# Kernel tuning notes

Measured on AMD Instinct MI355X. Metric: run time of the kernel, lower is better.

Reference implementation:

```python
import jax, jax.numpy as jnp
import numpy as np

B, N, HID, H = 2, 2048, 2048, 16
DH = HID // H  # 128


def _rope_tables(n, d, base=10000.0):
    inv_freq = 1.0 / (base ** (np.arange(0, d, 2, dtype=np.float32) / d))
    t = np.arange(n, dtype=np.float32)
    freqs = np.outer(t, inv_freq)                 # [N, d/2]
    emb = np.concatenate([freqs, freqs], axis=-1)  # [N, d]
    return jnp.asarray(np.cos(emb)), jnp.asarray(np.sin(emb))


def setup_inputs() -> dict:
    key = jax.random.key(0)
    k1, k2, k3 = jax.random.split(key, 3)
    std = 1.0 / HID ** 0.5
    cos, sin = _rope_tables(N, DH)
    return {
        "hidden_states": jax.random.normal(k1, (B, N, HID), dtype=jnp.float32),
        "cos": cos,
        "sin": sin,
        "w_qkv": (jax.random.truncated_normal(k2, -2.0, 2.0, (3 * HID, HID), jnp.float32) * std),
        "w_o": (jax.random.truncated_normal(k3, -2.0, 2.0, (HID, HID), jnp.float32) * std),
    }


def _rotate_half(x):
    d = x.shape[-1] // 2
    return jnp.concatenate([-x[..., d:], x[..., :d]], axis=-1)


def reference(hidden_states, cos, sin, w_qkv, w_o):
    b, n, _ = hidden_states.shape
    qkv = (hidden_states @ w_qkv.T).reshape(b, n, 3, H, DH)
    q, k, v = qkv[:, :, 0], qkv[:, :, 1], qkv[:, :, 2]  # [B,N,H,DH]
    c = cos[:, None, :]  # [N,1,DH] broadcasts over heads
    s = sin[:, None, :]
    q = q * c + _rotate_half(q) * s
    k = k * c + _rotate_half(k) * s
    scale = 1.0 / jnp.sqrt(jnp.asarray(DH, q.dtype))
    scores = jnp.einsum("bqhd,bkhd->bhqk", q, k) * scale
    attn = jax.nn.softmax(scores, axis=-1)
    out = jnp.einsum("bhqk,bkhd->bqhd", attn, v).reshape(b, n, HID)
    return out @ w_o.T
```

## Files before the change

### kernel.cpp

```cpp
#include <hip/hip_runtime.h>
#include <math.h>

#define NB 2
#define NN 2048
#define HIDDEN 2048
#define NHEAD 16
#define DHEAD 128

typedef __attribute__((ext_vector_type(8))) short bf16x8;
typedef __attribute__((ext_vector_type(4))) float floatx4;

static __device__ __forceinline__ short f2bf(float f) {
    union { float f; unsigned u; } v; v.f = f;
    unsigned r = v.u + 0x7fffu + ((v.u >> 16) & 1u);
    return (short)(r >> 16);
}
static __device__ __forceinline__ void gload_lds16(const short* g, short* l) {
    __builtin_amdgcn_global_load_lds(
        (const __attribute__((address_space(1))) void*)g,
        (__attribute__((address_space(3))) void*)l, 16, 0, 0);
}

__global__ __launch_bounds__(256) void cast_bf16_3(
    const float* __restrict__ a, const float* __restrict__ b, const float* __restrict__ c,
    short* __restrict__ oa, short* __restrict__ ob, short* __restrict__ oc,
    int n4a, int n4b, int n4c)
{
    int i = blockIdx.x * 256 + threadIdx.x;
    const float* s; short* d; int j;
    if (i < n4a) { s = a; d = oa; j = i; }
    else if (i < n4a + n4b) { s = b; d = ob; j = i - n4a; }
    else if (i < n4a + n4b + n4c) { s = c; d = oc; j = i - n4a - n4b; }
    else return;
    float4 v = ((const float4*)s)[j];
    short4 o;
    o.x = f2bf(v.x); o.y = f2bf(v.y); o.z = f2bf(v.z); o.w = f2bf(v.w);
    ((short4*)d)[j] = o;
}

__global__ __launch_bounds__(512, 2) void gemm_qkv_256x128(
    const short* __restrict__ A, const short* __restrict__ Bw,
    const float* __restrict__ cosT, const float* __restrict__ sinT,
    short* __restrict__ Qp, short* __restrict__ Kp, short* __restrict__ Vtp)
{
    __shared__ __align__(16) short AB[49152];

    const int tid = threadIdx.x;
    const int w = tid >> 6;
    const int l = tid & 63;
    const int quad = l >> 4;
    const int l15 = l & 15;
    const int bn = blockIdx.x * 128;
    const int bm = blockIdx.y * 256;
    const int K = HIDDEN;

    const short* src[6];
    int ldst[6];
#pragma unroll
    for (int ld = 0; ld < 2; ++ld) {
        int chunk = ld * 512 + tid;
        int row = chunk >> 3;
        int j = (chunk & 7) ^ (row & 7);
        int coff = j * 8;
        src[ld]     = A + (size_t)(bm + row) * K + coff;
        src[2 + ld] = A + (size_t)(bm + 128 + row) * K + coff;
        ldst[ld]     = chunk * 16;
        ldst[2 + ld] = 16384 + chunk * 16;
    }
    {
        int row = tid >> 3;
        int j = (tid & 7) ^ (row & 7);
        int coff = j * 8;
        src[4] = Bw + (size_t)(bn + row) * K + coff;
        src[5] = Bw + (size_t)(bn + 64 + row) * K + coff;
        ldst[4] = 32768 + tid * 16;
        ldst[5] = 32768 + 8192 + tid * 16;
    }

    const int xj = l15 & 7;
    const int jq0 = ((0 * 4 + quad) ^ xj) * 16;
    const int jq1 = ((1 * 4 + quad) ^ xj) * 16;
    const int arow = (w * 32 + l15) * 128;
    const int brow = 32768 + l15 * 128;

    floatx4 acc[2][8];
#pragma unroll
    for (int i = 0; i < 2; ++i)
#pragma unroll
        for (int j = 0; j < 8; ++j) acc[i][j] = (floatx4){0.f, 0.f, 0.f, 0.f};

#pragma unroll
    for (int i = 0; i < 6; ++i)
        gload_lds16(src[i], (short*)((char*)AB + ldst[i]));

#define STAGE(i) gload_lds16(src[i] + kpf, (short*)((char*)AB + ldst[i] + so))
#define MFMA(d, x, y) d = __builtin_amdgcn_mfma_f32_16x16x32_bf16(x, y, d, 0, 0, 0)

    const int NT = K / 64;
#pragma unroll 1
    for (int t = 0; t < NT; ++t) {
        const int co = (t & 1) * 49152;
        const int so = co ^ 49152;
        int kpf = (t + 1) * 64;
        if (kpf == K) kpf = 0;

        bf16x8 a[2][2], b[4][2];

        asm volatile("s_waitcnt vmcnt(1)" ::: "memory");
        __builtin_amdgcn_s_barrier();
#pragma unroll
        for (int m = 0; m < 2; ++m) {
            a[m][0] = *(const bf16x8*)((const char*)AB + co + arow + m * 2048 + jq0);
            a[m][1] = *(const bf16x8*)((const char*)AB + co + arow + m * 2048 + jq1);
        }
#pragma unroll
        for (int n = 0; n < 4; ++n) {
            b[n][0] = *(const bf16x8*)((const char*)AB + co + brow + n * 2048 + jq0);
            b[n][1] = *(const bf16x8*)((const char*)AB + co + brow + n * 2048 + jq1);
        }
        STAGE(0); STAGE(1); STAGE(2); STAGE(3); STAGE(4);
        __builtin_amdgcn_s_setprio(1);
#pragma unroll
        for (int m = 0; m < 2; ++m)
#pragma unroll
            for (int n = 0; n < 4; ++n) {
                MFMA(acc[m][n], a[m][0], b[n][0]);
                MFMA(acc[m][n], a[m][1], b[n][1]);
            }
        __builtin_amdgcn_s_setprio(0);

        asm volatile("s_waitcnt vmcnt(5)" ::: "memory");
        __builtin_amdgcn_s_barrier();
#pragma unroll
        for (int n = 0; n < 4; ++n) {
            b[n][0] = *(const bf16x8*)((const char*)AB + co + brow + (4 + n) * 2048 + jq0);
            b[n][1] = *(const bf16x8*)((const char*)AB + co + brow + (4 + n) * 2048 + jq1);
        }
        STAGE(5);
        __builtin_amdgcn_s_setprio(1);
#pragma unroll
        for (int m = 0; m < 2; ++m)
#pragma unroll
            for (int n = 0; n < 4; ++n) {
                MFMA(acc[m][4 + n], a[m][0], b[n][0]);
                MFMA(acc[m][4 + n], a[m][1], b[n][1]);
            }
        __builtin_amdgcn_s_setprio(0);
    }
#undef STAGE
#undef MFMA

    asm volatile("s_waitcnt vmcnt(0)" ::: "memory");

    const int which = bn >> 11;
    const int head = (bn >> 7) & (NHEAD - 1);
    const float qsc = (which == 0) ? 0.12751791525f : 1.0f;

#pragma unroll
    for (int m = 0; m < 2; ++m) {
#pragma unroll
        for (int reg = 0; reg < 4; ++reg) {
            int gm = bm + w * 32 + m * 16 + quad * 4 + reg;
            int b2 = gm >> 11, nseq = gm & (NN - 1);
            int bh = b2 * NHEAD + head;
            if (which == 2) {
#pragma unroll
                for (int n = 0; n < 8; ++n) {
                    int d = n * 16 + l15;
                    Vtp[((size_t)bh * DHEAD + d) * NN + nseq] = f2bf(acc[m][n][reg]);
                }
            } else {
                short* dst = (which == 0 ? Qp : Kp) + ((size_t)bh * NN + nseq) * DHEAD;
#pragma unroll
                for (int p = 0; p < 4; ++p) {
                    int d0 = p * 16 + l15;
                    float c = cosT[(size_t)nseq * DHEAD + d0];
                    float s = sinT[(size_t)nseq * DHEAD + d0];
                    float e0 = acc[m][p][reg];
                    float e1 = acc[m][p + 4][reg];
                    dst[d0]      = f2bf((e0 * c - e1 * s) * qsc);
                    dst[d0 + 64] = f2bf((e1 * c + e0 * s) * qsc);
                }
            }
        }
    }
}

template <int MODE>
__global__ __launch_bounds__(256) void gemm_bf16_nt(
    const short* __restrict__ A, const short* __restrict__ Bw,
    const float* __restrict__ cosT, const float* __restrict__ sinT,
    short* __restrict__ Qp, short* __restrict__ Kp, short* __restrict__ Vtp,
    float* __restrict__ Cp, int M, int N, int K)
{
    __shared__ __align__(16) short AB[1280 * 8];

    const int tid = threadIdx.x;
    const int w = tid >> 6;
    const int l = tid & 63;
    const int quad = l >> 4;
    const int l15 = l & 15;
    const int bm = blockIdx.y * 128;
    const int bn = blockIdx.x * 128;

    const int wm = (w & 1) * 64;
    const int wn2 = w >> 1;

    const short* gptr[5];
    short* lptr[5];
#pragma unroll
    for (int r5 = 0; r5 < 5; ++r5) {
        int s = r5 * 256 + tid;
        int m = (s < 640) ? s : s - 640;
        int row = m / 5;
        int ch = m - row * 5;
        if (ch == 4) ch = 0;
        gptr[r5] = ((s < 640) ? (A + (size_t)(bm + row) * K)
                              : (Bw + (size_t)(bn + row) * K)) + ch * 8;
        lptr[r5] = &AB[s * 8];
    }

    floatx4 acc[4][4];
#pragma unroll
    for (int i = 0; i < 4; ++i)
#pragma unroll
        for (int j = 0; j < 4; ++j) acc[i][j] = (floatx4){0.f, 0.f, 0.f, 0.f};

    for (int k0 = 0; k0 < K; k0 += 32) {
        __syncthreads();
#pragma unroll
        for (int r5 = 0; r5 < 5; ++r5)
            gload_lds16(gptr[r5] + k0, lptr[r5]);
        __syncthreads();

        bf16x8 af[4], bf[4];
#pragma unroll
        for (int i = 0; i < 4; ++i)
            af[i] = *(const bf16x8*)&AB[((wm + i * 16 + l15) * 5 + quad) * 8];
#pragma unroll
        for (int j = 0; j < 4; ++j) {
            int col = wn2 * 32 + (j & 1) * 16 + ((j >> 1) << 6);
            bf[j] = *(const bf16x8*)&AB[(640 + (col + l15) * 5 + quad) * 8];
        }
#pragma unroll
        for (int i = 0; i < 4; ++i)
#pragma unroll
            for (int j = 0; j < 4; ++j)
                acc[i][j] = __builtin_amdgcn_mfma_f32_16x16x32_bf16(af[i], bf[j], acc[i][j], 0, 0, 0);
    }

    if (MODE == 1) {
#pragma unroll
        for (int i = 0; i < 4; ++i) {
#pragma unroll
            for (int reg = 0; reg < 4; ++reg) {
                int row = bm + wm + i * 16 + quad * 4 + reg;
                float* crow = Cp + (size_t)row * N + bn;
#pragma unroll
                for (int j = 0; j < 4; ++j)
                    crow[wn2 * 32 + (j & 1) * 16 + ((j >> 1) << 6) + l15] = acc[i][j][reg];
            }
        }
    } else {
        const int which = bn >> 11;
        const int head = (bn >> 7) & (NHEAD - 1);
        const float qsc = (which == 0) ? 0.12751791525f : 1.0f;
#pragma unroll
        for (int i = 0; i < 4; ++i) {
#pragma unroll
            for (int reg = 0; reg < 4; ++reg) {
                int m = bm + wm + i * 16 + quad * 4 + reg;
                int b = m >> 11, n = m & (NN - 1);
                int bh = b * NHEAD + head;
                if (which == 2) {
#pragma unroll
                    for (int j = 0; j < 4; ++j) {
                        int d = wn2 * 32 + (j & 1) * 16 + ((j >> 1) << 6) + l15;
                        Vtp[((size_t)bh * DHEAD + d) * NN + n] = f2bf(acc[i][j][reg]);
                    }
                } else {
                    short* dst = (which == 0 ? Qp : Kp) + ((size_t)bh * NN + n) * DHEAD;
#pragma unroll
                    for (int j = 0; j < 2; ++j) {
                        int d0 = wn2 * 32 + j * 16 + l15;
                        float c = cosT[(size_t)n * DHEAD + d0];
                        float s = sinT[(size_t)n * DHEAD + d0];
                        float e0 = acc[i][j][reg], e1 = acc[i][j + 2][reg];
                        dst[d0]      = f2bf((e0 * c - e1 * s) * qsc);
                        dst[d0 + 64] = f2bf((e1 * c + e0 * s) * qsc);
                    }
                }
            }
        }
    }
}

__global__ __launch_bounds__(256, 2) void attn_mfma(
    const short* __restrict__ Qb, const short* __restrict__ Kb,
    const short* __restrict__ Vt, short* __restrict__ AOb)
{
    __shared__ __align__(16) short Ks[64 * 128];
    __shared__ __align__(16) short Vs[128 * 64];
    __shared__ __align__(16) short Ps[4][32][72];

    const int tid = threadIdx.x;
    const int w = tid >> 6;
    const int l = tid & 63;
    const int quad = l >> 4;
    const int l15 = l & 15;
    const int bh = blockIdx.y;
    const int qt = blockIdx.x * 128;

    const short* Qg = Qb + (size_t)bh * NN * DHEAD;
    const short* Kg = Kb + (size_t)bh * NN * DHEAD;
    const short* Vg = Vt + (size_t)bh * DHEAD * NN;

    bf16x8 qf[2][4];
#pragma unroll
    for (int mi = 0; mi < 2; ++mi) {
        const short* qrow = Qg + (size_t)(qt + w * 32 + mi * 16 + l15) * DHEAD + quad * 8;
#pragma unroll
        for (int kc = 0; kc < 4; ++kc) qf[mi][kc] = *(const bf16x8*)(qrow + kc * 32);
    }

    floatx4 of[2][8];
#pragma unroll
    for (int mi = 0; mi < 2; ++mi)
#pragma unroll
        for (int dc = 0; dc < 8; ++dc) of[mi][dc] = (floatx4){0.f, 0.f, 0.f, 0.f};
    float ls[2][4] = {{0.f, 0.f, 0.f, 0.f}, {0.f, 0.f, 0.f, 0.f}};

    for (int kt = 0; kt < NN; kt += 64) {
        __syncthreads();
#pragma unroll
        for (int rr = 0; rr < 4; ++rr) {
            int s = (w * 4 + rr) * 64 + l;
            int row = s >> 4;
            int j = (s & 15) ^ (row & 15);
            gload_lds16(Kg + (size_t)(kt + row) * DHEAD + j * 8, &Ks[s * 8]);
        }
#pragma unroll
        for (int rr = 0; rr < 4; ++rr) {
            int s = (w * 4 + rr) * 64 + l;
            int row = s >> 3;
            int c = (s & 7) ^ (row & 7);
            gload_lds16(Vg + (size_t)row * NN + kt + c * 8, &Vs[s * 8]);
        }
        __syncthreads();

        floatx4 sf[2][4];
#pragma unroll
        for (int n16 = 0; n16 < 4; ++n16) {
            bf16x8 kf[4];
            const short* kbase = &Ks[(n16 * 16 + l15) * 128];
#pragma unroll
            for (int kc = 0; kc < 4; ++kc)
                kf[kc] = *(const bf16x8*)&kbase[((4 * kc + quad) ^ l15) * 8];
#pragma unroll
            for (int mi = 0; mi < 2; ++mi) {
                floatx4 acc = (floatx4){0.f, 0.f, 0.f, 0.f};
#pragma unroll
                for (int kc = 0; kc < 4; ++kc)
                    acc = __builtin_amdgcn_mfma_f32_16x16x32_bf16(qf[mi][kc], kf[kc], acc, 0, 0, 0);
                sf[mi][n16] = acc;
            }
        }

#pragma unroll
        for (int mi = 0; mi < 2; ++mi)
#pragma unroll
            for (int n16 = 0; n16 < 4; ++n16)
#pragma unroll
                for (int r = 0; r < 4; ++r) {
                    float p = exp2f(sf[mi][n16][r]);
                    ls[mi][r] += p;
                    Ps[w][mi * 16 + quad * 4 + r][n16 * 16 + l15] = f2bf(p);
                }

        bf16x8 pa[2][2];
#pragma unroll
        for (int mi = 0; mi < 2; ++mi)
#pragma unroll
            for (int kc = 0; kc < 2; ++kc)
                pa[mi][kc] = *(const bf16x8*)&Ps[w][mi * 16 + l15][kc * 32 + quad * 8];

#pragma unroll
        for (int dc = 0; dc < 8; ++dc) {
            int row = dc * 16 + l15;
#pragma unroll
            for (int kc = 0; kc < 2; ++kc) {
                bf16x8 vf = *(const bf16x8*)&Vs[row * 64 + (((kc * 4 + quad) ^ (row & 7)) * 8)];
#pragma unroll
                for (int mi = 0; mi < 2; ++mi)
                    of[mi][dc] = __builtin_amdgcn_mfma_f32_16x16x32_bf16(
                                     pa[mi][kc], vf, of[mi][dc], 0, 0, 0);
            }
        }
    }

    const int b = bh >> 4, h = bh & (NHEAD - 1);
#pragma unroll
    for (int mi = 0; mi < 2; ++mi)
#pragma unroll
        for (int r = 0; r < 4; ++r) {
            float s = ls[mi][r];
            s += __shfl_xor(s, 1, 64);
            s += __shfl_xor(s, 2, 64);
            s += __shfl_xor(s, 4, 64);
            s += __shfl_xor(s, 8, 64);
            float inv = 1.0f / s;
            int row = qt + w * 32 + mi * 16 + quad * 4 + r;
            short* dst = AOb + ((size_t)(b * NN + row)) * HIDDEN + h * DHEAD;
#pragma unroll
            for (int dc = 0; dc < 8; ++dc)
                dst[dc * 16 + l15] = f2bf(of[mi][dc][r] * inv);
        }
}

extern "C" void kernel_launch(void* const* d_in, const int* in_sizes, int n_in,
                              void* d_out, int out_size, void* d_ws, size_t ws_size,
                              hipStream_t stream)
{
    const float* hs = (const float*)d_in[0];
    const float* cosT = (const float*)d_in[1];
    const float* sinT = (const float*)d_in[2];
    const float* wqkv = (const float*)d_in[3];
    const float* wo = (const float*)d_in[4];
    float* out = (float*)d_out;

    const size_t N_HS = (size_t)NB * NN * HIDDEN;
    const size_t N_WQ = (size_t)3 * HIDDEN * HIDDEN;
    const size_t N_WO = (size_t)HIDDEN * HIDDEN;
    const size_t SZ = (size_t)NB * NHEAD * NN * DHEAD;

    short* Ahs   = (short*)d_ws;
    short* Wqkvb = Ahs + N_HS;
    short* Wob   = Wqkvb + N_WQ;
    short* Qb    = Wob + N_WO;
    short* Kb    = Qb + SZ;
    short* Vtb   = Kb + SZ;
    short* AOb   = Vtb + SZ;

    {
        int n4a = (int)(N_HS / 4), n4b = (int)(N_WQ / 4), n4c = (int)(N_WO / 4);
        int total = n4a + n4b + n4c;
        cast_bf16_3<<<(total + 255) / 256, 256, 0, stream>>>(
            hs, wqkv, wo, Ahs, Wqkvb, Wob, n4a, n4b, n4c);
    }
    {
        dim3 grid(3 * HIDDEN / 128, NB * NN / 256);
        gemm_qkv_256x128<<<grid, 512, 0, stream>>>(
            Ahs, Wqkvb, cosT, sinT, Qb, Kb, Vtb);
    }
    {
        dim3 grid(NN / 128, NB * NHEAD);
        attn_mfma<<<grid, 256, 0, stream>>>(Qb, Kb, Vtb, AOb);
    }
    {
        dim3 grid(HIDDEN / 128, NB * NN / 128);
        gemm_bf16_nt<1><<<grid, 256, 0, stream>>>(
            AOb, Wob, nullptr, nullptr, nullptr, nullptr, nullptr, out,
            NB * NN, HIDDEN, HIDDEN);
    }
}
```

Baseline: 433.9 us.

## Double-buffer K/V tiles and widen attention blocks to eight waves

The attention kernel now runs 8 waves per block over 256 query rows, so each K/V tile loaded into LDS is shared by twice as many queries. K and V tiles are double-buffered: the next tile's async global-to-LDS loads are issued before computing on the current one, with a single waitcnt+barrier per iteration replacing two syncthreads. This aims to hide load latency and halve K/V traffic per query, at the cost of more LDS per block (about 100KB), which may limit occupancy to one block per CU and halves the grid size to 256 blocks.

```diff
diff --git a/kernel.cpp b/kernel.cpp
--- a/kernel.cpp
+++ b/kernel.cpp
@@ -295,13 +295,13 @@
     }
 }
 
-__global__ __launch_bounds__(256, 2) void attn_mfma(
+__global__ __launch_bounds__(512, 2) void attn_mfma8(
     const short* __restrict__ Qb, const short* __restrict__ Kb,
     const short* __restrict__ Vt, short* __restrict__ AOb)
 {
-    __shared__ __align__(16) short Ks[64 * 128];
-    __shared__ __align__(16) short Vs[128 * 64];
-    __shared__ __align__(16) short Ps[4][32][72];
+    __shared__ __align__(16) short Ks[2][64 * 128];
+    __shared__ __align__(16) short Vs[2][128 * 64];
+    __shared__ __align__(16) short Ps[8][32][72];
 
     const int tid = threadIdx.x;
     const int w = tid >> 6;
@@ -309,7 +309,7 @@
     const int quad = l >> 4;
     const int l15 = l & 15;
     const int bh = blockIdx.y;
-    const int qt = blockIdx.x * 128;
+    const int qt = blockIdx.x * 256;
 
     const short* Qg = Qb + (size_t)bh * NN * DHEAD;
     const short* Kg = Kb + (size_t)bh * NN * DHEAD;
@@ -323,6 +323,25 @@
         for (int kc = 0; kc < 4; ++kc) qf[mi][kc] = *(const bf16x8*)(qrow + kc * 32);
     }
 
+    const short* ksrc[2]; int kdst[2];
+    const short* vsrc[2]; int vdst[2];
+#pragma unroll
+    for (int rr = 0; rr < 2; ++rr) {
+        int s = rr * 512 + tid;
+        {
+            int row = s >> 4;
+            int j = (s & 15) ^ (row & 15);
+            ksrc[rr] = Kg + (size_t)row * DHEAD + j * 8;
+            kdst[rr] = s * 8;
+        }
+        {
+            int row = s >> 3;
+            int c = (s & 7) ^ (row & 7);
+            vsrc[rr] = Vg + (size_t)row * NN + c * 8;
+            vdst[rr] = s * 8;
+        }
+    }
+
     floatx4 of[2][8];
 #pragma unroll
     for (int mi = 0; mi < 2; ++mi)
@@ -330,29 +349,33 @@
         for (int dc = 0; dc < 8; ++dc) of[mi][dc] = (floatx4){0.f, 0.f, 0.f, 0.f};
     float ls[2][4] = {{0.f, 0.f, 0.f, 0.f}, {0.f, 0.f, 0.f, 0.f}};
 
+#pragma unroll
+    for (int rr = 0; rr < 2; ++rr) {
+        gload_lds16(ksrc[rr], &Ks[0][0] + kdst[rr]);
+        gload_lds16(vsrc[rr], &Vs[0][0] + vdst[rr]);
+    }
+    asm volatile("s_waitcnt vmcnt(0)" ::: "memory");
+    __builtin_amdgcn_s_barrier();
+
+    int cur = 0;
+#pragma unroll 1
     for (int kt = 0; kt < NN; kt += 64) {
-        __syncthreads();
-#pragma unroll
-        for (int rr = 0; rr < 4; ++rr) {
-            int s = (w * 4 + rr) * 64 + l;
-            int row = s >> 4;
-            int j = (s & 15) ^ (row & 15);
-            gload_lds16(Kg + (size_t)(kt + row) * DHEAD + j * 8, &Ks[s * 8]);
-        }
-#pragma unroll
-        for (int rr = 0; rr < 4; ++rr) {
-            int s = (w * 4 + rr) * 64 + l;
-            int row = s >> 3;
-            int c = (s & 7) ^ (row & 7);
-            gload_lds16(Vg + (size_t)row * NN + kt + c * 8, &Vs[s * 8]);
-        }
-        __syncthreads();
+        if (kt + 64 < NN) {
+            const int nxt = cur ^ 1;
+#pragma unroll
+            for (int rr = 0; rr < 2; ++rr) {
+                gload_lds16(ksrc[rr] + (size_t)(kt + 64) * DHEAD, &Ks[nxt][0] + kdst[rr]);
+                gload_lds16(vsrc[rr] + (kt + 64), &Vs[nxt][0] + vdst[rr]);
+            }
+        }
+        const short* kb = &Ks[cur][0];
+        const short* vb = &Vs[cur][0];
 
         floatx4 sf[2][4];
 #pragma unroll
         for (int n16 = 0; n16 < 4; ++n16) {
             bf16x8 kf[4];
-            const short* kbase = &Ks[(n16 * 16 + l15) * 128];
+            const short* kbase = kb + (n16 * 16 + l15) * 128;
 #pragma unroll
             for (int kc = 0; kc < 4; ++kc)
                 kf[kc] = *(const bf16x8*)&kbase[((4 * kc + quad) ^ l15) * 8];
@@ -389,13 +412,17 @@
             int row = dc * 16 + l15;
 #pragma unroll
             for (int kc = 0; kc < 2; ++kc) {
-                bf16x8 vf = *(const bf16x8*)&Vs[row * 64 + (((kc * 4 + quad) ^ (row & 7)) * 8)];
+                bf16x8 vf = *(const bf16x8*)&vb[row * 64 + (((kc * 4 + quad) ^ (row & 7)) * 8)];
 #pragma unroll
                 for (int mi = 0; mi < 2; ++mi)
                     of[mi][dc] = __builtin_amdgcn_mfma_f32_16x16x32_bf16(
                                      pa[mi][kc], vf, of[mi][dc], 0, 0, 0);
             }
         }
+
+        asm volatile("s_waitcnt vmcnt(0)" ::: "memory");
+        __builtin_amdgcn_s_barrier();
+        cur ^= 1;
     }
 
     const int b = bh >> 4, h = bh & (NHEAD - 1);
@@ -453,8 +480,8 @@
             Ahs, Wqkvb, cosT, sinT, Qb, Kb, Vtb);
     }
     {
-        dim3 grid(NN / 128, NB * NHEAD);
-        attn_mfma<<<grid, 256, 0, stream>>>(Qb, Kb, Vtb, AOb);
+        dim3 grid(NN / 256, NB * NHEAD);
+        attn_mfma8<<<grid, 512, 0, stream>>>(Qb, Kb, Vtb, AOb);
     }
     {
         dim3 grid(HIDDEN / 128, NB * NN / 128);
```

Result: faster. 409.1 us (-5.7%).
